# Optimization experiments

Hardware: AMD Instinct MI355X
Metric: run time of the kernel (lower is better)

## Reference

```python
import jax, jax.numpy as jnp
import numpy as np

B, S, H, NH = 2, 2048, 2048, 16
HD = H // NH


def setup_inputs() -> dict:
    key = jax.random.key(0)
    ks = jax.random.split(key, 10)
    s = 1.0 / np.sqrt(H)
    x = jax.random.normal(ks[0], (B, S, H), dtype=jnp.float32)
    # additive causal mask: 0 on/below diagonal, -1e9 above
    causal = jnp.tril(jnp.ones((S, S), dtype=bool))
    mask = jnp.where(causal, 0.0, -1e9).astype(jnp.float32)[None, None]
    return {
        "x": x,
        "mask": mask,
        "wq": jax.random.normal(ks[1], (H, H), jnp.float32) * s,
        "bq": jnp.zeros((H,), jnp.float32),
        "wk": jax.random.normal(ks[2], (H, H), jnp.float32) * s,
        "bk": jnp.zeros((H,), jnp.float32),
        "wv": jax.random.normal(ks[3], (H, H), jnp.float32) * s,
        "bv": jnp.zeros((H,), jnp.float32),
        "wo": jax.random.normal(ks[4], (H, H), jnp.float32) * s,
        "bo": jnp.zeros((H,), jnp.float32),
    }


def reference(x, mask, wq, bq, wk, bk, wv, bv, wo, bo):
    b, s, _ = x.shape
    scale = HD ** (-0.5)
    # projections -> [b, nh, s, hd]
    def split_heads(t):
        return t.reshape(b, s, NH, HD).transpose(0, 2, 1, 3)
    q = split_heads(x @ wq + bq)
    k = split_heads(x @ wk + bk)
    v = split_heads(x @ wv + bv)
    scores = jnp.einsum('bhqd,bhkd->bhqk', q, k) * scale + mask
    attn = jax.nn.softmax(scores, axis=-1)
    out = jnp.einsum('bhqk,bhkd->bhqd', attn, v)
    out = out.transpose(0, 2, 1, 3).reshape(b, s, H)
    return out @ wo + bo
```

## Files before the change

kernel.cpp:

```cpp
#include <hip/hip_runtime.h>


using bf16x8 = __attribute__((ext_vector_type(8))) short;
using bf16x4 = __attribute__((ext_vector_type(4))) short;
using f32x4  = __attribute__((ext_vector_type(4))) float;

#define S_LEN 2048
#define NHEAD 16
#define HDIM  128
#define HID   2048

__device__ __forceinline__ unsigned short f2bf(float f) {
    unsigned int u = __float_as_uint(f);
    u += 0x7fffu + ((u >> 16) & 1u);
    return (unsigned short)(u >> 16);
}
__device__ __forceinline__ void gl2lds16(const void* g, void* l) {
    __builtin_amdgcn_global_load_lds(
        (const __attribute__((address_space(1))) void*)g,
        (__attribute__((address_space(3))) void*)l, 16, 0, 0);
}

__device__ __forceinline__ f32x4 pv_mfma(bf16x4 a, bf16x4 b, f32x4 c) {
#if defined(__HIP_DEVICE_COMPILE__)
#if __has_builtin(__builtin_amdgcn_mfma_f32_16x16x16bf16_1k)
    return __builtin_amdgcn_mfma_f32_16x16x16bf16_1k(a, b, c, 0, 0, 0);
#else
    asm("v_mfma_f32_16x16x16_bf16 %0, %1, %2, %0" : "+v"(c) : "v"(a), "v"(b));
    return c;
#endif
#else
    (void)a; (void)b;
    return c;
#endif
}

__global__ void convert_x(const float* __restrict__ x, unsigned short* __restrict__ xb) {
    int i = (blockIdx.x * 256 + threadIdx.x) * 4;
    float4 v = *(const float4*)(x + i);
    ushort4 o;
    o.x = f2bf(v.x); o.y = f2bf(v.y); o.z = f2bf(v.z); o.w = f2bf(v.w);
    *(ushort4*)(xb + i) = o;
}

__global__ void convert_wt(const float* __restrict__ w0, const float* __restrict__ w1,
                           const float* __restrict__ w2, const float* __restrict__ w3,
                           unsigned short* __restrict__ t0, unsigned short* __restrict__ t1,
                           unsigned short* __restrict__ t2, unsigned short* __restrict__ t3) {
    __shared__ float tile[64][65];
    int z = blockIdx.z;
    const float* src = (z == 0) ? w0 : (z == 1) ? w1 : (z == 2) ? w2 : w3;
    unsigned short* dst = (z == 0) ? t0 : (z == 1) ? t1 : (z == 2) ? t2 : t3;
    int r0 = blockIdx.y * 64, c0 = blockIdx.x * 64;
    int t = threadIdx.x;
    for (int i = t; i < 64 * 64; i += 256) {
        int r = i >> 6, c = i & 63;
        tile[r][c] = src[(size_t)(r0 + r) * HID + c0 + c];
    }
    __syncthreads();
    for (int i = t; i < 64 * 64; i += 256) {
        int r = i & 63, c = i >> 6;
        dst[(size_t)(c0 + c) * HID + r0 + r] = f2bf(tile[r][c]);
    }
}

__device__ __forceinline__ void sched0() { __builtin_amdgcn_sched_barrier(0); }
__device__ __forceinline__ void w_lgkm4() { asm volatile("s_waitcnt lgkmcnt(4)" ::: "memory"); sched0(); }
__device__ __forceinline__ void w_lgkm0() { asm volatile("s_waitcnt lgkmcnt(0)" ::: "memory"); sched0(); }
template <int NJ> __device__ __forceinline__ void w_lgkm_4nj() {
    if constexpr (NJ == 3) { asm volatile("s_waitcnt lgkmcnt(7)" ::: "memory"); }
    else                   { asm volatile("s_waitcnt lgkmcnt(6)" ::: "memory"); }
    sched0();
}
template <int NJ> __device__ __forceinline__ void w_vm_ns() {
    if constexpr (NJ == 3) { asm volatile("s_waitcnt vmcnt(7)" ::: "memory"); }
    else                   { asm volatile("s_waitcnt vmcnt(6)" ::: "memory"); }
    sched0();
}
__device__ __forceinline__ void w_vm2() { asm volatile("s_waitcnt vmcnt(2)" ::: "memory"); sched0(); }
__device__ __forceinline__ void w_vm0() { asm volatile("s_waitcnt vmcnt(0)" ::: "memory"); sched0(); }
__device__ __forceinline__ void barx() {
    asm volatile("" ::: "memory");
    __builtin_amdgcn_s_barrier();
    asm volatile("" ::: "memory");
}

template <int MODE, int NJ>
__launch_bounds__(512, 2)
__global__ void gemmT(const unsigned short* __restrict__ A,
                      const unsigned short* __restrict__ Bt0,
                      const float* __restrict__ bias0,
                      const float* __restrict__ bias1,
                      const float* __restrict__ bias2,
                      unsigned short* __restrict__ C0,
                      unsigned short* __restrict__ C1,
                      unsigned short* __restrict__ C2,
                      float* __restrict__ Cf) {
    constexpr int BN = NJ * 64;
    __shared__ __align__(16) unsigned short lds[2 * 16384 + 2 * NJ * 4096];
    unsigned short* const A0 = lds;
    unsigned short* const A1 = lds + 16384;
    unsigned short* const B0 = lds + 32768;
    unsigned short* const B1 = lds + 32768 + NJ * 4096;

    const int CPX = (MODE == 1) ? 64 : 32;
    int vb = (blockIdx.x & 7) * CPX + (blockIdx.x >> 3);
    int m0  = (vb & 15) * 256;
    int n0g = (vb >> 4) * BN;

    int tid = threadIdx.x;
    int lane = tid & 63;
    int wv_ = tid >> 6;
    int wr = wv_ >> 2, wc = wv_ & 3;
    int l15 = lane & 15, quad = lane >> 4;

    int tr = tid >> 3;
    int tc = ((tid & 7) ^ (tr & 7)) << 3;
    const unsigned short* gA = A   + (size_t)(m0  + tr) * HID + tc;
    const unsigned short* gB = Bt0 + (size_t)(n0g + tr) * HID + tc;
    const int td8 = tid * 8;

    int arow0 = (wr * 128 + l15) * 64;
    int brow0 = (wc * (16 * NJ) + l15) * 64;
    int sw0 = ((quad ^ (l15 & 7)) << 3);
    int sw1 = (((4 + quad) ^ (l15 & 7)) << 3);

    f32x4 acc[8][NJ];
#pragma unroll
    for (int i = 0; i < 8; ++i)
#pragma unroll
        for (int j = 0; j < NJ; ++j) acc[i][j] = (f32x4){0.f, 0.f, 0.f, 0.f};

    bf16x8 aX[4], aY[4], b0v[NJ], b1v[NJ];

#define STAGE(kt, AD, BD) do { int _kc = (kt) * 64;                          \
    gl2lds16(gA + _kc,             (AD) + td8);                              \
    gl2lds16(gA + 64 * HID + _kc,  (AD) + 4096 + td8);                       \
    gl2lds16(gA + 128 * HID + _kc, (AD) + 8192 + td8);                       \
    gl2lds16(gA + 192 * HID + _kc, (AD) + 12288 + td8);                      \
    _Pragma("unroll")                                                        \
    for (int _r = 0; _r < NJ; ++_r)                                          \
        gl2lds16(gB + (size_t)(_r * 64) * HID + _kc, (BD) + _r * 4096 + td8); } while (0)

#define LDA4(dst, AD, QB, SW) do {                                           \
    dst[0] = *(const bf16x8*)((AD) + arow0 + ((QB) + 0) * 1024 + (SW));      \
    dst[1] = *(const bf16x8*)((AD) + arow0 + ((QB) + 1) * 1024 + (SW));      \
    dst[2] = *(const bf16x8*)((AD) + arow0 + ((QB) + 2) * 1024 + (SW));      \
    dst[3] = *(const bf16x8*)((AD) + arow0 + ((QB) + 3) * 1024 + (SW)); } while (0)

#define LDB(dst, BD, SW) do {                                                \
    _Pragma("unroll")                                                        \
    for (int _n = 0; _n < NJ; ++_n)                                          \
        dst[_n] = *(const bf16x8*)((BD) + brow0 + _n * 1024 + (SW)); } while (0)

#define MF(Q, a, b) do {                                                     \
    __builtin_amdgcn_s_setprio(1);                                           \
    _Pragma("unroll")                                                        \
    for (int mi = 0; mi < 4; ++mi)                                           \
        _Pragma("unroll")                                                    \
        for (int nj = 0; nj < NJ; ++nj)                                      \
            acc[(Q) * 4 + mi][nj] =                                          \
                __builtin_amdgcn_mfma_f32_16x16x32_bf16(a[mi], b[nj],        \
                                                        acc[(Q) * 4 + mi][nj], 0, 0, 0); \
    __builtin_amdgcn_s_setprio(0); } while (0)

#define TILE(AD, BD, AN, BN_, ks) do {                                       \
    LDA4(aY, AD, 4, sw0);                                      \
    w_lgkm4();                                   \
    MF(0, aX, b0v);                                                          \
    LDA4(aX, AD, 0, sw1);                                                    \
    LDB(b1v, BD, sw1);                                   \
    w_lgkm_4nj<NJ>();                                          \
    MF(1, aY, b0v);                                                          \
    LDA4(aY, AD, 4, sw1);                                      \
    w_lgkm4();                                             \
    MF(0, aX, b1v);                                                          \
    w_lgkm0();                                \
    barx();                              \
    STAGE(ks, AD, BD);                          \
    w_vm_ns<NJ>();                        \
    barx();                                  \
    LDA4(aX, AN, 0, sw0);                                                    \
    LDB(b0v, BN_, sw0);                   \
    sched0();                                                                \
    MF(1, aY, b1v);                          \
} while (0)

    STAGE(0, A0, B0);
    STAGE(1, A1, B1);
    w_vm_ns<NJ>();
    barx();
    LDA4(aX, A0, 0, sw0);
    LDB(b0v, B0, sw0);

    for (int t = 0; t < 32; t += 2) {
        TILE(A0, B0, A1, B1, (t + 2 < 32) ? t + 2 : 31);
        TILE(A1, B1, A0, B0, (t + 3 < 32) ? t + 3 : 31);
    }
    asm volatile("s_waitcnt vmcnt(0) lgkmcnt(0)" ::: "memory");

#undef TILE
#undef STAGE
#undef LDA4
#undef LDB
#undef MF

#pragma unroll
    for (int j = 0; j < NJ; ++j) {
        int n = n0g + wc * (16 * NJ) + j * 16 + l15;
        int zj = (MODE == 1) ? (n >> 11) : 0;
        int nn = (MODE == 1) ? (n & 2047) : n;
        float bn = (MODE == 1)
                     ? ((zj == 0) ? bias0[nn] : (zj == 1) ? bias1[nn] : bias2[nn])
                     : bias0[nn];
        unsigned short* Cz = (zj == 0) ? C0 : (zj == 1) ? C1 : C2;
#pragma unroll
        for (int i = 0; i < 8; ++i) {
            int mb = m0 + wr * 128 + i * 16 + quad * 4;
            if (MODE == 1 && zj == 2) {
                int b = mb >> 11, s = mb & 2047, h = nn >> 7, d = nn & 127;
                int kt = s >> 4, qv = (s >> 2) & 3, ct = d >> 4, lv = d & 15;
                size_t addr = ((((size_t)((b << 4) + h) * 128 + kt) * 4 + (ct >> 1)) * 4 + qv) * 128
                              + lv * 8 + (ct & 1) * 4;
                ushort4 o;
                o.x = f2bf(acc[i][j][0] + bn);
                o.y = f2bf(acc[i][j][1] + bn);
                o.z = f2bf(acc[i][j][2] + bn);
                o.w = f2bf(acc[i][j][3] + bn);
                *(ushort4*)&Cz[addr] = o;
            } else {
#pragma unroll
                for (int reg = 0; reg < 4; ++reg) {
                    int m = mb + reg;
                    float v = acc[i][j][reg] + bn;
                    if (MODE == 0) {
                        Cf[(size_t)m * HID + nn] = v;
                    } else {
                        int b = m >> 11, s = m & 2047, h = nn >> 7, d = nn & 127;
                        if (zj == 1) {
                            int kt = s >> 4, lk = s & 15, kk = d >> 5, qk = (d >> 3) & 3, e = d & 7;
                            size_t addr = ((((size_t)((b << 4) + h) * 128 + kt) * 4 + kk) * 4 + qk) * 128
                                          + lk * 8 + e;
                            Cz[addr] = f2bf(v);
                        } else {
                            Cz[(size_t)(((b << 4) + h) * S_LEN + s) * HDIM + d] = f2bf(v);
                        }
                    }
                }
            }
        }
    }
}

__launch_bounds__(256, 2)
__global__ void attn_kernel(const unsigned short* __restrict__ Qg,
                            const unsigned short* __restrict__ Kp,
                            const unsigned short* __restrict__ Vp,
                            unsigned short* __restrict__ O) {
    __shared__ __align__(16) unsigned short kv[2][4096];

    int linear = blockIdx.x;
    int xcd = linear & 7;
    int u = linear >> 3;
    int bh = xcd * 4 + (u & 3);
    int q = u >> 2;
    int b = bh >> 4, h = bh & 15;

    int tid = threadIdx.x, lane = tid & 63, w = tid >> 6;
    int l15 = lane & 15, quad = lane >> 4;

    const unsigned short* Qb = Qg + (size_t)bh * (S_LEN * HDIM);
    const unsigned short* Kg = Kp + (size_t)bh * 262144;
    const unsigned short* Vg = Vp + (size_t)bh * 262144;
    const float k2 = 0.08838834764831845f * 1.4426950408889634f;

    const int frag = quad * 128 + l15 * 8;
    const int td8 = tid * 8;

#define VLO(x) __builtin_shufflevector(x, x, 0, 1, 2, 3)
#define VHI(x) __builtin_shufflevector(x, x, 4, 5, 6, 7)
#define ASTAGE(kt, bf) do { size_t _g = (size_t)(kt) * 2048 + td8;             \
    gl2lds16(Kg + _g, &kv[bf][td8]);                                           \
    gl2lds16(Vg + _g, &kv[bf][2048 + td8]); } while (0)

    auto run_qblock = [&](int qb) {
        int s  = 4 * qb + w;
        int r0 = s * 16;
        int N  = 4 * qb + 4;

        bf16x8 qf[4];
#pragma unroll
        for (int kk = 0; kk < 4; ++kk)
            qf[kk] = *(const bf16x8*)&Qb[(size_t)(r0 + l15) * HDIM + kk * 32 + quad * 8];

        f32x4 o_acc[8];
#pragma unroll
        for (int c = 0; c < 8; ++c) o_acc[c] = (f32x4){0.f, 0.f, 0.f, 0.f};
        float l_part = 0.f;

        ASTAGE(0, 0);
        for (int kt = 0; kt < N; ++kt) {
            int nk = (kt + 1 < N) ? kt + 1 : kt;
            ASTAGE(nk, (kt + 1) & 1);
            w_vm2();
            barx();

            const unsigned short* KL = &kv[kt & 1][frag];
            const unsigned short* VL = &kv[kt & 1][2048 + frag];
            bf16x8 kb0 = *(const bf16x8*)(KL);
            bf16x8 kb1 = *(const bf16x8*)(KL + 512);
            bf16x8 kb2 = *(const bf16x8*)(KL + 1024);
            bf16x8 kb3 = *(const bf16x8*)(KL + 1536);
            bf16x8 v0 = *(const bf16x8*)(VL);
            bf16x8 v1 = *(const bf16x8*)(VL + 512);
            bf16x8 v2 = *(const bf16x8*)(VL + 1024);
            bf16x8 v3 = *(const bf16x8*)(VL + 1536);

            f32x4 st0 = (f32x4){0.f, 0.f, 0.f, 0.f};
            f32x4 st1 = (f32x4){0.f, 0.f, 0.f, 0.f};
            __builtin_amdgcn_s_setprio(1);
            st0 = __builtin_amdgcn_mfma_f32_16x16x32_bf16(kb0, qf[0], st0, 0, 0, 0);
            st1 = __builtin_amdgcn_mfma_f32_16x16x32_bf16(kb1, qf[1], st1, 0, 0, 0);
            st0 = __builtin_amdgcn_mfma_f32_16x16x32_bf16(kb2, qf[2], st0, 0, 0, 0);
            st1 = __builtin_amdgcn_mfma_f32_16x16x32_bf16(kb3, qf[3], st1, 0, 0, 0);
            __builtin_amdgcn_s_setprio(0);
            f32x4 stv = st0 + st1;

            float p0, p1, p2, p3;
            int doff = kt - s;
            if (doff >= 0) {
                int d16 = doff << 4;
                p0 = (d16 + quad * 4 + 0 <= l15) ? exp2f(stv[0] * k2) : 0.f;
                p1 = (d16 + quad * 4 + 1 <= l15) ? exp2f(stv[1] * k2) : 0.f;
                p2 = (d16 + quad * 4 + 2 <= l15) ? exp2f(stv[2] * k2) : 0.f;
                p3 = (d16 + quad * 4 + 3 <= l15) ? exp2f(stv[3] * k2) : 0.f;
            } else {
                p0 = exp2f(stv[0] * k2); p1 = exp2f(stv[1] * k2);
                p2 = exp2f(stv[2] * k2); p3 = exp2f(stv[3] * k2);
            }
            l_part += (p0 + p1) + (p2 + p3);

            bf16x4 pf;
            pf[0] = (short)f2bf(p0); pf[1] = (short)f2bf(p1);
            pf[2] = (short)f2bf(p2); pf[3] = (short)f2bf(p3);

            __builtin_amdgcn_s_setprio(1);
            o_acc[0] = pv_mfma(pf, VLO(v0), o_acc[0]);
            o_acc[1] = pv_mfma(pf, VHI(v0), o_acc[1]);
            o_acc[2] = pv_mfma(pf, VLO(v1), o_acc[2]);
            o_acc[3] = pv_mfma(pf, VHI(v1), o_acc[3]);
            o_acc[4] = pv_mfma(pf, VLO(v2), o_acc[4]);
            o_acc[5] = pv_mfma(pf, VHI(v2), o_acc[5]);
            o_acc[6] = pv_mfma(pf, VLO(v3), o_acc[6]);
            o_acc[7] = pv_mfma(pf, VHI(v3), o_acc[7]);
            __builtin_amdgcn_s_setprio(0);
            barx();
        }
        w_vm0();
        barx();

        float lp = l_part;
        lp += __shfl_xor(lp, 16, 64);
        lp += __shfl_xor(lp, 32, 64);
#pragma unroll
        for (int reg = 0; reg < 4; ++reg) {
            float l = __shfl(lp, quad * 4 + reg, 64);
            float inv = 1.f / l;
            int srow = r0 + quad * 4 + reg;
            unsigned short* op = O + (size_t)(b * S_LEN + srow) * HID + h * HDIM;
#pragma unroll
            for (int ct = 0; ct < 8; ++ct)
                op[ct * 16 + l15] = f2bf(o_acc[ct][reg] * inv);
        }
    };

    run_qblock(q);
    run_qblock(31 - q);

#undef ASTAGE
#undef VLO
#undef VHI
}

extern "C" void kernel_launch(void* const* d_in, const int* in_sizes, int n_in,
                              void* d_out, int out_size, void* d_ws, size_t ws_size,
                              hipStream_t stream) {
    (void)in_sizes; (void)n_in; (void)out_size; (void)ws_size;
    const float* x  = (const float*)d_in[0];
    const float* wq = (const float*)d_in[2];
    const float* bq = (const float*)d_in[3];
    const float* wk = (const float*)d_in[4];
    const float* bk = (const float*)d_in[5];
    const float* wv = (const float*)d_in[6];
    const float* bv = (const float*)d_in[7];
    const float* wo = (const float*)d_in[8];
    const float* bo = (const float*)d_in[9];
    float* out = (float*)d_out;

    unsigned short* ws = (unsigned short*)d_ws;
    const size_t WSZ = 4194304;
    unsigned short* wqT = ws;
    unsigned short* wkT = ws + WSZ;
    unsigned short* wvT = ws + 2 * WSZ;
    unsigned short* woT = ws + 3 * WSZ;
    unsigned short* xb  = ws + 4 * WSZ;
    unsigned short* Ab  = ws + 4 * WSZ;
    unsigned short* Qb  = ws + 6 * WSZ;
    unsigned short* Kb  = ws + 8 * WSZ;
    unsigned short* Vb  = ws + 10 * WSZ;

    convert_x<<<dim3(8192), 256, 0, stream>>>(x, xb);
    convert_wt<<<dim3(32, 32, 4), 256, 0, stream>>>(wq, wk, wv, wo, wqT, wkT, wvT, woT);
    gemmT<1, 3><<<dim3(512), 512, 0, stream>>>(xb, wqT, bq, bk, bv,
                                               Qb, Kb, Vb, nullptr);
    attn_kernel<<<dim3(512), 256, 0, stream>>>(Qb, Kb, Vb, Ab);
    gemmT<0, 2><<<dim3(256), 512, 0, stream>>>(Ab, woT, bo, nullptr, nullptr,
                                               nullptr, nullptr, nullptr, out);
}
```

Measured before the change: 394.7 us.

## Use 256x256 eight-phase pipelined QKV GEMM and merge conversion kernels

Replaces the templated QKV projection GEMM with a dedicated kernel using 256x256 output tiles, split into four quarter-MFMA phases per k-tile. Each phase interleaves LDS reads, global-to-LDS staging of half-tiles and barriers. The larger tile should raise arithmetic intensity and cut the grid from 512 to 384 blocks, while finer-grained staging overlaps loads with compute. It also fuses the x conversion and weight transpose into one launch to remove a kernel launch. The tradeoffs are more barriers per iteration, 128 KB of LDS per block, which limits occupancy, and heavier register use for the 8x4 accumulator array.

```diff
diff --git a/kernel.cpp b/kernel.cpp
--- a/kernel.cpp
+++ b/kernel.cpp
@@ -35,20 +35,23 @@
 #endif
 }
 
-__global__ void convert_x(const float* __restrict__ x, unsigned short* __restrict__ xb) {
-    int i = (blockIdx.x * 256 + threadIdx.x) * 4;
-    float4 v = *(const float4*)(x + i);
-    ushort4 o;
-    o.x = f2bf(v.x); o.y = f2bf(v.y); o.z = f2bf(v.z); o.w = f2bf(v.w);
-    *(ushort4*)(xb + i) = o;
-}
-
-__global__ void convert_wt(const float* __restrict__ w0, const float* __restrict__ w1,
-                           const float* __restrict__ w2, const float* __restrict__ w3,
-                           unsigned short* __restrict__ t0, unsigned short* __restrict__ t1,
-                           unsigned short* __restrict__ t2, unsigned short* __restrict__ t3) {
+__global__ void convert_all(const float* __restrict__ x,
+                            const float* __restrict__ w0, const float* __restrict__ w1,
+                            const float* __restrict__ w2, const float* __restrict__ w3,
+                            unsigned short* __restrict__ xb,
+                            unsigned short* __restrict__ t0, unsigned short* __restrict__ t1,
+                            unsigned short* __restrict__ t2, unsigned short* __restrict__ t3) {
+    int z = blockIdx.z;
+    if (z >= 4) {
+        int lin = (z - 4) * 1024 + blockIdx.y * 32 + blockIdx.x;
+        int i = (lin * 256 + threadIdx.x) * 4;
+        float4 v = *(const float4*)(x + i);
+        ushort4 o;
+        o.x = f2bf(v.x); o.y = f2bf(v.y); o.z = f2bf(v.z); o.w = f2bf(v.w);
+        *(ushort4*)(xb + i) = o;
+        return;
+    }
     __shared__ float tile[64][65];
-    int z = blockIdx.z;
     const float* src = (z == 0) ? w0 : (z == 1) ? w1 : (z == 2) ? w2 : w3;
     unsigned short* dst = (z == 0) ? t0 : (z == 1) ? t1 : (z == 2) ? t2 : t3;
     int r0 = blockIdx.y * 64, c0 = blockIdx.x * 64;
@@ -65,18 +68,11 @@
 }
 
 __device__ __forceinline__ void sched0() { __builtin_amdgcn_sched_barrier(0); }
+__device__ __forceinline__ void w_lgkm8() { asm volatile("s_waitcnt lgkmcnt(8)" ::: "memory"); sched0(); }
 __device__ __forceinline__ void w_lgkm4() { asm volatile("s_waitcnt lgkmcnt(4)" ::: "memory"); sched0(); }
 __device__ __forceinline__ void w_lgkm0() { asm volatile("s_waitcnt lgkmcnt(0)" ::: "memory"); sched0(); }
-template <int NJ> __device__ __forceinline__ void w_lgkm_4nj() {
-    if constexpr (NJ == 3) { asm volatile("s_waitcnt lgkmcnt(7)" ::: "memory"); }
-    else                   { asm volatile("s_waitcnt lgkmcnt(6)" ::: "memory"); }
-    sched0();
-}
-template <int NJ> __device__ __forceinline__ void w_vm_ns() {
-    if constexpr (NJ == 3) { asm volatile("s_waitcnt vmcnt(7)" ::: "memory"); }
-    else                   { asm volatile("s_waitcnt vmcnt(6)" ::: "memory"); }
-    sched0();
-}
+__device__ __forceinline__ void w_vm6() { asm volatile("s_waitcnt vmcnt(6)" ::: "memory"); sched0(); }
+__device__ __forceinline__ void w_vm4() { asm volatile("s_waitcnt vmcnt(4)" ::: "memory"); sched0(); }
 __device__ __forceinline__ void w_vm2() { asm volatile("s_waitcnt vmcnt(2)" ::: "memory"); sched0(); }
 __device__ __forceinline__ void w_vm0() { asm volatile("s_waitcnt vmcnt(0)" ::: "memory"); sched0(); }
 __device__ __forceinline__ void barx() {
@@ -85,28 +81,207 @@
     asm volatile("" ::: "memory");
 }
 
-template <int MODE, int NJ>
 __launch_bounds__(512, 2)
-__global__ void gemmT(const unsigned short* __restrict__ A,
+__global__ void gemm8p(const unsigned short* __restrict__ A,
+                       const unsigned short* __restrict__ Bt,
+                       const float* __restrict__ bias0,
+                       const float* __restrict__ bias1,
+                       const float* __restrict__ bias2,
+                       unsigned short* __restrict__ C0,
+                       unsigned short* __restrict__ C1,
+                       unsigned short* __restrict__ C2) {
+    __shared__ __align__(16) unsigned short lds[65536];
+    unsigned short* const A0 = lds;
+    unsigned short* const A1 = lds + 16384;
+    unsigned short* const B0 = lds + 32768;
+    unsigned short* const B1 = lds + 49152;
+
+    int vb = (blockIdx.x & 7) * 48 + (blockIdx.x >> 3);
+    int m0  = (vb & 15) * 256;
+    int n0g = (vb >> 4) * 256;
+    int z   = n0g >> 11;
+    int nb0 = n0g & 2047;
+
+    int tid = threadIdx.x;
+    int lane = tid & 63;
+    int wv_ = tid >> 6;
+    int wr = wv_ >> 2, wc = wv_ & 3;
+    int l15 = lane & 15, quad = lane >> 4;
+
+    int tr = tid >> 3;
+    int tc = ((tid & 7) ^ (tr & 7)) << 3;
+    const unsigned short* gA = A  + (size_t)(m0  + tr) * HID + tc;
+    const unsigned short* gB = Bt + (size_t)(n0g + tr) * HID + tc;
+    const int td8 = tid * 8;
+
+    int arow0 = (wr * 128 + l15) * 64;
+    int brow0 = (wc * 64 + l15) * 64;
+    int swz[2] = { ((quad ^ (l15 & 7)) << 3), (((4 + quad) ^ (l15 & 7)) << 3) };
+
+    f32x4 acc[8][4];
+#pragma unroll
+    for (int i = 0; i < 8; ++i)
+#pragma unroll
+        for (int j = 0; j < 4; ++j) acc[i][j] = (f32x4){0.f, 0.f, 0.f, 0.f};
+
+    bf16x8 av[2][4];
+    bf16x8 bv[2][2][2];
+
+#define SGA(kt, half, AD) do {                                               \
+    size_t _g = (size_t)((half) * 128) * HID + (size_t)(kt) * 64;            \
+    gl2lds16(gA + _g,            (AD) + (half) * 8192 + td8);                \
+    gl2lds16(gA + _g + 64 * HID, (AD) + (half) * 8192 + 4096 + td8); } while (0)
+
+#define SGB(kt, half, BD) do {                                               \
+    size_t _g = (size_t)((half) * 128) * HID + (size_t)(kt) * 64;            \
+    gl2lds16(gB + _g,            (BD) + (half) * 8192 + td8);                \
+    gl2lds16(gB + _g + 64 * HID, (BD) + (half) * 8192 + 4096 + td8); } while (0)
+
+#define RDAV(AD, hm) do {                                                    \
+    _Pragma("unroll")                                                        \
+    for (int kk = 0; kk < 2; ++kk)                                           \
+        _Pragma("unroll")                                                    \
+        for (int mi = 0; mi < 4; ++mi)                                       \
+            av[kk][mi] = *(const bf16x8*)((AD) + arow0 + (hm) * 4096         \
+                                          + mi * 1024 + swz[kk]); } while (0)
+
+#define RDBV(BD, hn) do {                                                    \
+    _Pragma("unroll")                                                        \
+    for (int kk = 0; kk < 2; ++kk)                                           \
+        _Pragma("unroll")                                                    \
+        for (int nj = 0; nj < 2; ++nj)                                       \
+            bv[hn][kk][nj] = *(const bf16x8*)((BD) + brow0 + (hn) * 2048     \
+                                              + nj * 1024 + swz[kk]); } while (0)
+
+#define MFQ(hm, hn) do {                                                     \
+    __builtin_amdgcn_s_setprio(1);                                           \
+    _Pragma("unroll")                                                        \
+    for (int kk = 0; kk < 2; ++kk)                                           \
+        _Pragma("unroll")                                                    \
+        for (int mi = 0; mi < 4; ++mi)                                       \
+            _Pragma("unroll")                                                \
+            for (int nj = 0; nj < 2; ++nj)                                   \
+                acc[(hm) * 4 + mi][(hn) * 2 + nj] =                          \
+                    __builtin_amdgcn_mfma_f32_16x16x32_bf16(av[kk][mi],      \
+                        bv[hn][kk][nj], acc[(hm) * 4 + mi][(hn) * 2 + nj],   \
+                        0, 0, 0);                                            \
+    __builtin_amdgcn_s_setprio(0); sched0(); } while (0)
+
+    SGA(0, 0, A0); SGA(0, 1, A0);
+    SGB(0, 0, B0); SGB(0, 1, B0);
+    SGA(1, 0, A1); SGB(1, 0, B1);
+    w_vm4();
+    barx();
+
+    for (int it = 0; it < 16; ++it) {
+        int t  = 2 * it;
+        int t2 = (t + 2 < 32) ? t + 2 : 31;
+        int t3 = (t + 3 < 32) ? t + 3 : 31;
+        RDAV(A0, 0); RDBV(B0, 0);
+        SGA(t + 1, 1, A1);
+        w_lgkm8();
+        barx(); w_lgkm0();
+        MFQ(0, 0);
+        barx();
+        RDBV(B0, 1);
+        SGB(t + 1, 1, B1);
+        barx(); w_lgkm0();
+        MFQ(0, 1);
+        barx();
+        RDAV(A0, 1);
+        SGA(t2, 0, A0);
+        barx(); w_lgkm0();
+        MFQ(1, 0);
+        barx();
+        SGB(t2, 0, B0);
+        barx();
+        MFQ(1, 1);
+        w_vm4();
+        barx();
+        RDAV(A1, 0); RDBV(B1, 0);
+        SGA(t2, 1, A0);
+        w_lgkm8();
+        barx(); w_lgkm0();
+        MFQ(0, 0);
+        barx();
+        RDBV(B1, 1);
+        SGB(t2, 1, B0);
+        barx(); w_lgkm0();
+        MFQ(0, 1);
+        barx();
+        RDAV(A1, 1);
+        SGA(t3, 0, A1);
+        barx(); w_lgkm0();
+        MFQ(1, 0);
+        barx();
+        SGB(t3, 0, B1);
+        barx();
+        MFQ(1, 1);
+        w_vm4();
+        barx();
+    }
+    asm volatile("s_waitcnt vmcnt(0) lgkmcnt(0)" ::: "memory");
+
+#undef SGA
+#undef SGB
+#undef RDAV
+#undef RDBV
+#undef MFQ
+
+#pragma unroll
+    for (int j = 0; j < 4; ++j) {
+        int n = nb0 + wc * 64 + j * 16 + l15;
+        float bn = (z == 0) ? bias0[n] : (z == 1) ? bias1[n] : bias2[n];
+        unsigned short* Cz = (z == 0) ? C0 : (z == 1) ? C1 : C2;
+#pragma unroll
+        for (int i = 0; i < 8; ++i) {
+            int mb = m0 + wr * 128 + i * 16 + quad * 4;
+            if (z == 2) {
+                int b = mb >> 11, s = mb & 2047, h = n >> 7, d = n & 127;
+                int kt = s >> 4, qv = (s >> 2) & 3, ct = d >> 4, lv = d & 15;
+                size_t addr = ((((size_t)((b << 4) + h) * 128 + kt) * 4 + (ct >> 1)) * 4 + qv) * 128
+                              + lv * 8 + (ct & 1) * 4;
+                ushort4 o;
+                o.x = f2bf(acc[i][j][0] + bn);
+                o.y = f2bf(acc[i][j][1] + bn);
+                o.z = f2bf(acc[i][j][2] + bn);
+                o.w = f2bf(acc[i][j][3] + bn);
+                *(ushort4*)&Cz[addr] = o;
+            } else {
+#pragma unroll
+                for (int reg = 0; reg < 4; ++reg) {
+                    int m = mb + reg;
+                    float v = acc[i][j][reg] + bn;
+                    int b = m >> 11, s = m & 2047, h = n >> 7, d = n & 127;
+                    if (z == 1) {
+                        int kt = s >> 4, lk = s & 15, kk = d >> 5, qk = (d >> 3) & 3, e = d & 7;
+                        size_t addr = ((((size_t)((b << 4) + h) * 128 + kt) * 4 + kk) * 4 + qk) * 128
+                                      + lk * 8 + e;
+                        Cz[addr] = f2bf(v);
+                    } else {
+                        Cz[(size_t)(((b << 4) + h) * S_LEN + s) * HDIM + d] = f2bf(v);
+                    }
+                }
+            }
+        }
+    }
+}
+
+__launch_bounds__(512, 2)
+__global__ void gemmO(const unsigned short* __restrict__ A,
                       const unsigned short* __restrict__ Bt0,
                       const float* __restrict__ bias0,
-                      const float* __restrict__ bias1,
-                      const float* __restrict__ bias2,
-                      unsigned short* __restrict__ C0,
-                      unsigned short* __restrict__ C1,
-                      unsigned short* __restrict__ C2,
                       float* __restrict__ Cf) {
-    constexpr int BN = NJ * 64;
+    constexpr int NJ = 2;
     __shared__ __align__(16) unsigned short lds[2 * 16384 + 2 * NJ * 4096];
     unsigned short* const A0 = lds;
     unsigned short* const A1 = lds + 16384;
     unsigned short* const B0 = lds + 32768;
     unsigned short* const B1 = lds + 32768 + NJ * 4096;
 
-    const int CPX = (MODE == 1) ? 64 : 32;
-    int vb = (blockIdx.x & 7) * CPX + (blockIdx.x >> 3);
+    int vb = (blockIdx.x & 7) * 32 + (blockIdx.x >> 3);
     int m0  = (vb & 15) * 256;
-    int n0g = (vb >> 4) * BN;
+    int n0g = (vb >> 4) * (NJ * 64);
 
     int tid = threadIdx.x;
     int lane = tid & 63;
@@ -165,30 +340,30 @@
     __builtin_amdgcn_s_setprio(0); } while (0)
 
 #define TILE(AD, BD, AN, BN_, ks) do {                                       \
-    LDA4(aY, AD, 4, sw0);                                      \
-    w_lgkm4();                                   \
+    LDA4(aY, AD, 4, sw0);                                                    \
+    w_lgkm4();                                                               \
     MF(0, aX, b0v);                                                          \
     LDA4(aX, AD, 0, sw1);                                                    \
-    LDB(b1v, BD, sw1);                                   \
-    w_lgkm_4nj<NJ>();                                          \
+    LDB(b1v, BD, sw1);                                                       \
+    asm volatile("s_waitcnt lgkmcnt(6)" ::: "memory"); sched0();             \
     MF(1, aY, b0v);                                                          \
-    LDA4(aY, AD, 4, sw1);                                      \
-    w_lgkm4();                                             \
+    LDA4(aY, AD, 4, sw1);                                                    \
+    w_lgkm4();                                                               \
     MF(0, aX, b1v);                                                          \
-    w_lgkm0();                                \
-    barx();                              \
-    STAGE(ks, AD, BD);                          \
-    w_vm_ns<NJ>();                        \
-    barx();                                  \
+    w_lgkm0();                                                               \
+    barx();                                                                  \
+    STAGE(ks, AD, BD);                                                       \
+    w_vm6();                                                                 \
+    barx();                                                                  \
     LDA4(aX, AN, 0, sw0);                                                    \
-    LDB(b0v, BN_, sw0);                   \
+    LDB(b0v, BN_, sw0);                                                      \
     sched0();                                                                \
-    MF(1, aY, b1v);                          \
+    MF(1, aY, b1v);                                                          \
 } while (0)
 
     STAGE(0, A0, B0);
     STAGE(1, A1, B1);
-    w_vm_ns<NJ>();
+    w_vm6();
     barx();
     LDA4(aX, A0, 0, sw0);
     LDB(b0v, B0, sw0);
@@ -208,45 +383,14 @@
 #pragma unroll
     for (int j = 0; j < NJ; ++j) {
         int n = n0g + wc * (16 * NJ) + j * 16 + l15;
-        int zj = (MODE == 1) ? (n >> 11) : 0;
-        int nn = (MODE == 1) ? (n & 2047) : n;
-        float bn = (MODE == 1)
-                     ? ((zj == 0) ? bias0[nn] : (zj == 1) ? bias1[nn] : bias2[nn])
-                     : bias0[nn];
-        unsigned short* Cz = (zj == 0) ? C0 : (zj == 1) ? C1 : C2;
+        float bn = bias0[n];
 #pragma unroll
         for (int i = 0; i < 8; ++i) {
             int mb = m0 + wr * 128 + i * 16 + quad * 4;
-            if (MODE == 1 && zj == 2) {
-                int b = mb >> 11, s = mb & 2047, h = nn >> 7, d = nn & 127;
-                int kt = s >> 4, qv = (s >> 2) & 3, ct = d >> 4, lv = d & 15;
-                size_t addr = ((((size_t)((b << 4) + h) * 128 + kt) * 4 + (ct >> 1)) * 4 + qv) * 128
-                              + lv * 8 + (ct & 1) * 4;
-                ushort4 o;
-                o.x = f2bf(acc[i][j][0] + bn);
-                o.y = f2bf(acc[i][j][1] + bn);
-                o.z = f2bf(acc[i][j][2] + bn);
-                o.w = f2bf(acc[i][j][3] + bn);
-                *(ushort4*)&Cz[addr] = o;
-            } else {
-#pragma unroll
-                for (int reg = 0; reg < 4; ++reg) {
-                    int m = mb + reg;
-                    float v = acc[i][j][reg] + bn;
-                    if (MODE == 0) {
-                        Cf[(size_t)m * HID + nn] = v;
-                    } else {
-                        int b = m >> 11, s = m & 2047, h = nn >> 7, d = nn & 127;
-                        if (zj == 1) {
-                            int kt = s >> 4, lk = s & 15, kk = d >> 5, qk = (d >> 3) & 3, e = d & 7;
-                            size_t addr = ((((size_t)((b << 4) + h) * 128 + kt) * 4 + kk) * 4 + qk) * 128
-                                          + lk * 8 + e;
-                            Cz[addr] = f2bf(v);
-                        } else {
-                            Cz[(size_t)(((b << 4) + h) * S_LEN + s) * HDIM + d] = f2bf(v);
-                        }
-                    }
-                }
+#pragma unroll
+            for (int reg = 0; reg < 4; ++reg) {
+                int m = mb + reg;
+                Cf[(size_t)m * HID + n] = acc[i][j][reg] + bn;
             }
         }
     }
@@ -409,11 +553,9 @@
     unsigned short* Kb  = ws + 8 * WSZ;
     unsigned short* Vb  = ws + 10 * WSZ;
 
-    convert_x<<<dim3(8192), 256, 0, stream>>>(x, xb);
-    convert_wt<<<dim3(32, 32, 4), 256, 0, stream>>>(wq, wk, wv, wo, wqT, wkT, wvT, woT);
-    gemmT<1, 3><<<dim3(512), 512, 0, stream>>>(xb, wqT, bq, bk, bv,
-                                               Qb, Kb, Vb, nullptr);
+    convert_all<<<dim3(32, 32, 12), 256, 0, stream>>>(x, wq, wk, wv, wo,
+                                                      xb, wqT, wkT, wvT, woT);
+    gemm8p<<<dim3(384), 512, 0, stream>>>(xb, wqT, bq, bk, bv, Qb, Kb, Vb);
     attn_kernel<<<dim3(512), 256, 0, stream>>>(Qb, Kb, Vb, Ab);
-    gemmT<0, 2><<<dim3(256), 512, 0, stream>>>(Ab, woT, bo, nullptr, nullptr,
-                                               nullptr, nullptr, nullptr, out);
-}
+    gemmO<<<dim3(256), 512, 0, stream>>>(Ab, woT, bo, out);
+}
```

After: 393.9 us. No clear change (-0.2%).
